# Kernel tuning notes

Measured on AMD Instinct MI355X. Metric: run time of the kernel, lower is better.

Reference implementation:

```python
import jax, jax.numpy as jnp
import numpy as np

B, N_CH, T, E = 64, 64, 1000, 512
KS = [3, 5, 7]
TC, AH, GC, HEADS, NCLS = 16, 32, 32, 4, 2
F3 = TC * len(KS)
EPS = 1e-5


def _gat(x, src, dst, W, a_src, a_dst, bias, N):
    # PyG GATConv, concat=False: h = x @ W.T -> [N, H, C]
    H, C = a_src.shape
    h = (x @ W.T).reshape(-1, H, C)
    al_s = (h * a_src).sum(-1)  # [N, H]
    al_d = (h * a_dst).sum(-1)
    e = al_s[src] + al_d[dst]  # [E, H]
    e = jnp.where(e > 0, e, 0.2 * e)  # leaky_relu(0.2)
    emax = jax.ops.segment_max(e, dst, num_segments=N)
    ex = jnp.exp(e - emax[dst])
    denom = jax.ops.segment_sum(ex, dst, num_segments=N)
    alpha = ex / denom[dst]
    out = jax.ops.segment_sum(h[src] * alpha[:, :, None], dst, num_segments=N)
    return out.mean(1) + bias  # concat=False -> head mean, then bias


def _branch(xr, cw, cb, g, b, m, v, w1, b1, w2, b2):
    k = cw.shape[-1]
    o = jax.lax.conv_general_dilated(xr, cw, (1,), [(k // 2, k // 2)],
                                     dimension_numbers=('NCH', 'OIH', 'NCH'))
    o = o + cb[None, :, None]
    o = (o - m[None, :, None]) / jnp.sqrt(v[None, :, None] + EPS) * g[None, :, None] + b[None, :, None]
    o = jax.nn.gelu(o, approximate=False)
    h = jnp.tanh(jnp.einsum('hc,nct->nht', w1, o) + b1[None, :, None])
    s = jnp.einsum('oh,nht->not', w2, h) + b2[None, :, None]  # [N,1,T]
    wts = jax.nn.softmax(s, axis=2)
    return (o * wts).sum(-1)  # [N, TC]


def reference(x, edge_index,
              conv_w_0, conv_b_0, bn_g_0, bn_b_0, bn_m_0, bn_v_0, aw1_0, ab1_0, aw2_0, ab2_0,
              conv_w_1, conv_b_1, bn_g_1, bn_b_1, bn_m_1, bn_v_1, aw1_1, ab1_1, aw2_1, ab2_1,
              conv_w_2, conv_b_2, bn_g_2, bn_b_2, bn_m_2, bn_v_2, aw1_2, ab1_2, aw2_2, ab2_2,
              se_w1, se_b1, se_w2, se_b2,
              gat1_w, gat1_asrc, gat1_adst, gat1_bias, bn1_g, bn1_b, bn1_m, bn1_v,
              skip_w, skip_b,
              gat2_w, gat2_asrc, gat2_adst, gat2_bias, bn2_g, bn2_b, bn2_m, bn2_v,
              fc_w, fc_b):
    Bx, n, Tn = x.shape
    xr = x.reshape(Bx * n, 1, Tn)
    branches = [
        (conv_w_0, conv_b_0, bn_g_0, bn_b_0, bn_m_0, bn_v_0, aw1_0, ab1_0, aw2_0, ab2_0),
        (conv_w_1, conv_b_1, bn_g_1, bn_b_1, bn_m_1, bn_v_1, aw1_1, ab1_1, aw2_1, ab2_1),
        (conv_w_2, conv_b_2, bn_g_2, bn_b_2, bn_m_2, bn_v_2, aw1_2, ab1_2, aw2_2, ab2_2),
    ]
    feats = [_branch(xr, *p) for p in branches]
    xf = jnp.concatenate(feats, axis=1)  # [B*n, F3]
    # SE block (squeeze over all nodes, per original mean over dim 0)
    sq = xf.mean(0, keepdims=True)
    sq = jax.nn.gelu(sq @ se_w1.T + se_b1, approximate=False)
    sq = jax.nn.sigmoid(sq @ se_w2.T + se_b2)
    xf = xf * sq
    # batched edge index + self loops (PyG GATConv default add_self_loops)
    offs = (jnp.arange(Bx) * n).astype(edge_index.dtype)
    src = (edge_index[0][None, :] + offs[:, None]).reshape(-1)
    dst = (edge_index[1][None, :] + offs[:, None]).reshape(-1)
    loops = jnp.arange(Bx * n, dtype=edge_index.dtype)
    src = jnp.concatenate([src, loops])
    dst = jnp.concatenate([dst, loops])
    Nn = Bx * n
    h1 = _gat(xf, src, dst, gat1_w, gat1_asrc, gat1_adst, gat1_bias, Nn)
    h1 = (h1 - bn1_m) / jnp.sqrt(bn1_v + EPS) * bn1_g + bn1_b
    h1 = jax.nn.gelu(h1 + xf @ skip_w.T + skip_b, approximate=False)
    h2 = _gat(h1, src, dst, gat2_w, gat2_asrc, gat2_adst, gat2_bias, Nn)
    h2 = (h2 - bn2_m) / jnp.sqrt(bn2_v + EPS) * bn2_g + bn2_b
    h2 = jax.nn.gelu(h2 + h1, approximate=False)
    pooled = h2.reshape(Bx, n, -1).mean(1)  # global_mean_pool per graph
    return pooled @ fc_w.T + fc_b


def setup_inputs() -> dict:
    key = jax.random.key(0)
    it = iter(jax.random.split(key, 80))
    nk = lambda *s: jax.random.normal(next(it), s, jnp.float32) * 0.1
    d = {}
    d['x'] = jax.random.normal(next(it), (B, N_CH, T), jnp.float32)
    s0 = jax.random.randint(next(it), (E,), 0, N_CH)
    off = jax.random.randint(next(it), (E,), 1, N_CH)
    d['edge_index'] = jnp.stack([s0, (s0 + off) % N_CH]).astype(jnp.int32)  # no self loops
    for i, k in enumerate(KS):
        d[f'conv_w_{i}'] = nk(TC, 1, k); d[f'conv_b_{i}'] = nk(TC)
        d[f'bn_g_{i}'] = 1.0 + nk(TC); d[f'bn_b_{i}'] = nk(TC)
        d[f'bn_m_{i}'] = nk(TC); d[f'bn_v_{i}'] = 1.0 + jnp.abs(nk(TC))
        d[f'aw1_{i}'] = nk(AH, TC); d[f'ab1_{i}'] = nk(AH)
        d[f'aw2_{i}'] = nk(1, AH); d[f'ab2_{i}'] = nk(1)
    d['se_w1'] = nk(F3 // 4, F3); d['se_b1'] = nk(F3 // 4)
    d['se_w2'] = nk(F3, F3 // 4); d['se_b2'] = nk(F3)
    d['gat1_w'] = nk(HEADS * GC, F3)
    d['gat1_asrc'] = nk(HEADS, GC); d['gat1_adst'] = nk(HEADS, GC); d['gat1_bias'] = nk(GC)
    d['bn1_g'] = 1.0 + nk(GC); d['bn1_b'] = nk(GC); d['bn1_m'] = nk(GC); d['bn1_v'] = 1.0 + jnp.abs(nk(GC))
    d['skip_w'] = nk(GC, F3); d['skip_b'] = nk(GC)
    d['gat2_w'] = nk(HEADS * GC, GC)
    d['gat2_asrc'] = nk(HEADS, GC); d['gat2_adst'] = nk(HEADS, GC); d['gat2_bias'] = nk(GC)
    d['bn2_g'] = 1.0 + nk(GC); d['bn2_b'] = nk(GC); d['bn2_m'] = nk(GC); d['bn2_v'] = 1.0 + jnp.abs(nk(GC))
    d['fc_w'] = nk(NCLS, GC); d['fc_b'] = nk(NCLS)
    return d
```

## Files before the change

kernel.cpp:

```cpp
#include <hip/hip_runtime.h>
#include <math.h>

#define N_NODES 4096
#define T_LEN 1000
#define TCH 16
#define AHD 32
#define F3D 48
#define GCD 32
#define NPG 64
#define NGRAPH 64
#define BN_EPS 1e-5f

typedef _Float16 half4_t __attribute__((ext_vector_type(4)));
typedef float float4_t __attribute__((ext_vector_type(4)));

__device__ __forceinline__ float fast_rcp(float x){ return __builtin_amdgcn_rcpf(x); }
__device__ __forceinline__ float gelu_exact(float v){
    return 0.5f*v*(1.0f+erff(v*0.70710678118654752f));
}

struct BranchParams {
    const float* conv_w; const float* conv_b;
    const float* bn_g; const float* bn_b; const float* bn_m; const float* bn_v;
    const float* aw1; const float* ab1; const float* aw2; const float* ab2;
    int K; int col0;
};

__global__ __launch_bounds__(256)
void branch_kernel(const float* __restrict__ x,
                   BranchParams bp0, BranchParams bp1, BranchParams bp2,
                   float* __restrict__ xf, float* __restrict__ colacc)
{
    __shared__ __align__(16) float xs_f[1056];
    __shared__ __align__(8)  _Float16 xsc[4][1048];
    __shared__ __align__(8)  _Float16 cws16[256];
    __shared__ float s_arr[1024];
    __shared__ __align__(16) float shiftc[16];
    __shared__ float scl[16];
    __shared__ float reds[4];
    __shared__ __align__(16) float fredw[4][16];

    const BranchParams bp = (blockIdx.y==0)? bp0 : (blockIdx.y==1)? bp1 : bp2;
    const int tid = threadIdx.x;
    const int node = blockIdx.x;
    const int K = bp.K;
    const float* xrow = x + (size_t)node*T_LEN;

    for (int j=tid;j<1056;j+=256){
        int q = j-8;
        xs_f[j] = (q>=0 && q<T_LEN)? xrow[q] : 0.f;
    }
    if (tid<16){
        float s = bp.bn_g[tid]*rsqrtf(bp.bn_v[tid]+BN_EPS);
        scl[tid]=s;
        shiftc[tid] = (bp.conv_b[tid]-bp.bn_m[tid])*s + bp.bn_b[tid];
    }
    __syncthreads();
    for (int j=tid;j<1048;j+=256){
        xsc[0][j]=(_Float16)xs_f[j];
        xsc[1][j]=(_Float16)xs_f[j+1];
        xsc[2][j]=(_Float16)xs_f[j+2];
        xsc[3][j]=(_Float16)xs_f[j+3];
    }
    {
        int ch=tid>>4, tap=tid&15;
        cws16[tid] = (tap<K)? (_Float16)(bp.conv_w[ch*K+tap]*scl[ch]) : (_Float16)0.f;
    }
    __syncthreads();

    const int lane = tid&63, wave = tid>>6;
    const int col  = lane&15;
    const int kg   = (lane>>4)<<2;

    const half4_t  acw = *(const half4_t*)&cws16[col*16+kg];
    const float4_t csh = *(const float4_t*)&shiftc[kg];

    const float TWO_LOG2E = 2.8853900817779268f;
    const float LOG2E = 1.4426950408889634f;

    float4_t wr0 = *(const float4_t*)&bp.aw1[(size_t)col*TCH + kg];
    float4_t wr1 = *(const float4_t*)&bp.aw1[(size_t)(col+16)*TCH + kg];
    half4_t a0,a1;
    #pragma unroll
    for (int r=0;r<4;r++){ a0[r]=(_Float16)(wr0[r]*TWO_LOG2E); a1[r]=(_Float16)(wr1[r]*TWO_LOG2E); }
    float4_t c0  = *(const float4_t*)&bp.ab1[kg];
    float4_t c1  = *(const float4_t*)&bp.ab1[16+kg];
    #pragma unroll
    for (int r=0;r<4;r++){ c0[r]*=TWO_LOG2E; c1[r]*=TWO_LOG2E; }
    float4_t w20 = *(const float4_t*)&bp.aw2[kg];
    float4_t w21 = *(const float4_t*)&bp.aw2[16+kg];
    #pragma unroll
    for (int r=0;r<4;r++){ w20[r]*=LOG2E; w21[r]*=LOG2E; }
    const float b2v = bp.ab2[0]*LOG2E;
    const float w2sum8 = w20[0]+w20[1]+w20[2]+w20[3]+w21[0]+w21[1]+w21[2]+w21[3];

    const float C1GE = -2.30220818f;
    const float C2GE = -0.10294324f;

    const int abase = 8 + wave*256 + col + kg - K/2;
    const int sh = abase & 3;
    const _Float16* xw_base = &xsc[sh][abase - sh];

    half4_t oreg[16];
    #pragma unroll
    for (int i=0;i<16;i++){
        half4_t xw = *(const half4_t*)(xw_base + i*16);
        float4_t d = __builtin_amdgcn_mfma_f32_16x16x16f16(acw, xw, csh, 0,0,0);

        float vv[4], dd[4];
        #pragma unroll
        for (int r=0;r<4;r++){
            float v = d[r];
            vv[r] = v;
            float t = fmaxf(v, -9.0f);
            float u = t*t;
            float pq = fmaf(C2GE, u, C1GE);
            dd[r] = __builtin_amdgcn_exp2f(pq*t) + 1.0f;
        }
        half4_t ob;
        {
            float rp0 = fast_rcp(dd[0]*dd[1]);
            float rp1 = fast_rcp(dd[2]*dd[3]);
            ob[0] = (_Float16)(vv[0]*(dd[1]*rp0));
            ob[1] = (_Float16)(vv[1]*(dd[0]*rp0));
            ob[2] = (_Float16)(vv[2]*(dd[3]*rp1));
            ob[3] = (_Float16)(vv[3]*(dd[2]*rp1));
        }
        oreg[i] = ob;

        float4_t h0 = __builtin_amdgcn_mfma_f32_16x16x16f16(a0, ob, c0, 0,0,0);
        float4_t h1 = __builtin_amdgcn_mfma_f32_16x16x16f16(a1, ob, c1, 0,0,0);
        float accr = 0.f;
        #pragma unroll
        for (int r=0;r<4;r++){
            float e0 = __builtin_amdgcn_exp2f(h0[r]) + 1.0f;
            float e1 = __builtin_amdgcn_exp2f(h1[r]) + 1.0f;
            float rp = fast_rcp(e0*e1);
            accr = fmaf(w20[r], e1*rp, accr);
            accr = fmaf(w21[r], e0*rp, accr);
        }
        float part = fmaf(-2.0f, accr, w2sum8);
        part += __shfl_xor(part,16);
        part += __shfl_xor(part,32);
        const int pos0 = wave*256 + i*16;
        if (lane<16) s_arr[pos0+lane] = (pos0+lane < T_LEN)? (part + b2v) : -INFINITY;
    }
    __syncthreads();

    float sv[4];
    #pragma unroll
    for (int ii=0;ii<4;ii++) sv[ii]=s_arr[tid+ii*256];
    float e[4]; float ls=0.f;
    #pragma unroll
    for (int ii=0;ii<4;ii++){ e[ii]=__builtin_amdgcn_exp2f(sv[ii]); ls+=e[ii]; }
    #pragma unroll
    for (int off=32;off;off>>=1) ls += __shfl_xor(ls,off);
    if (lane==0) reds[wave]=ls;
    __syncthreads();
    const float invS = fast_rcp(reds[0]+reds[1]+reds[2]+reds[3]);
    #pragma unroll
    for (int ii=0;ii<4;ii++) s_arr[tid+ii*256]=e[ii];
    __syncthreads();

    half4_t acch = {(_Float16)0.f,(_Float16)0.f,(_Float16)0.f,(_Float16)0.f};
    #pragma unroll
    for (int i=0;i<16;i++){
        _Float16 eh = (_Float16)s_arr[wave*256 + i*16 + col];
        half4_t evv = {eh,eh,eh,eh};
        acch += oreg[i]*evv;
    }
    {
        union { half4_t h; unsigned u[2]; } au, bu;
        au.h = acch;
        #pragma unroll
        for (int off=1;off<16;off<<=1){
            bu.u[0] = __shfl_xor(au.u[0], off);
            bu.u[1] = __shfl_xor(au.u[1], off);
            au.h += bu.h;
        }
        if (col==0){
            float4_t accf;
            #pragma unroll
            for (int r=0;r<4;r++) accf[r] = (float)au.h[r];
            *(float4_t*)&fredw[wave][kg] = accf;
        }
    }
    __syncthreads();
    if (tid<16){
        float v = (fredw[0][tid]+fredw[1][tid]+fredw[2][tid]+fredw[3][tid])*invS;
        xf[(size_t)node*F3D + bp.col0 + tid] = v;
        atomicAdd(&colacc[bp.col0 + tid], v);
    }
}

__global__ __launch_bounds__(128)
void csr_local_kernel(const int* __restrict__ ei, int epg,
                      int* __restrict__ rowstart, int* __restrict__ cols){
    __shared__ int deg[64], cur[64], rs[65];
    const int tid = threadIdx.x;
    if (tid<64) deg[tid]=0;
    __syncthreads();
    const int total = epg + 64;
    for (int e=tid;e<total;e+=128){
        int d = (e<epg)? ei[epg+e] : (e-epg);
        atomicAdd(&deg[d],1);
    }
    __syncthreads();
    if (tid<64){
        int v = deg[tid];
        int s = v;
        #pragma unroll
        for (int off=1;off<64;off<<=1){
            int t = __shfl_up(s, off);
            if (tid >= off) s += t;
        }
        rs[tid+1] = s;
        if (tid==0) rs[0]=0;
        cur[tid] = s - v;
    }
    __syncthreads();
    for (int e=tid;e<total;e+=128){
        int sN,dN;
        if (e<epg){ sN=ei[e]; dN=ei[epg+e]; } else { sN=dN=e-epg; }
        int pos = atomicAdd(&cur[dN],1);
        cols[pos]=sN;
    }
    if (tid<65) rowstart[tid]=rs[tid];
}

__global__ __launch_bounds__(512)
void gat_tail_kernel(const int* __restrict__ rowstart, const int* __restrict__ cols,
                     const float* __restrict__ xf, const float* __restrict__ colacc,
                     const float* __restrict__ se_w1, const float* __restrict__ se_b1,
                     const float* __restrict__ se_w2, const float* __restrict__ se_b2,
                     const float* __restrict__ W1,
                     const float* __restrict__ asrc1, const float* __restrict__ adst1,
                     const float* __restrict__ bias1,
                     const float* __restrict__ bn1_g, const float* __restrict__ bn1_b,
                     const float* __restrict__ bn1_m, const float* __restrict__ bn1_v,
                     const float* __restrict__ skip_w, const float* __restrict__ skip_b,
                     const float* __restrict__ W2,
                     const float* __restrict__ asrc2, const float* __restrict__ adst2,
                     const float* __restrict__ bias2,
                     const float* __restrict__ bn2_g, const float* __restrict__ bn2_b,
                     const float* __restrict__ bn2_m, const float* __restrict__ bn2_v,
                     const float* __restrict__ fc_w, const float* __restrict__ fc_b,
                     float* __restrict__ out)
{
    __shared__ float hb[64*128];
    __shared__ float xh[64*48];
    __shared__ float h1l[64*32];
    __shared__ float a1s[256], a1d[256], a2s[256], a2d[256];
    __shared__ float skw[32*48];
    __shared__ float poolv[32];
    __shared__ float cm[F3D], g1[12], gate_sh[F3D];

    const int g = blockIdx.x;
    const int tid = threadIdx.x;
    const int n0 = g*NPG;

    if (tid<F3D) cm[tid]=colacc[tid]*(1.0f/(float)N_NODES);
    __syncthreads();
    if (tid<12){
        float v=se_b1[tid];
        for (int j=0;j<F3D;j++) v += se_w1[tid*F3D+j]*cm[j];
        g1[tid]=gelu_exact(v);
    }
    __syncthreads();
    if (tid<F3D){
        float v=se_b2[tid];
        for (int m2=0;m2<12;m2++) v += se_w2[tid*12+m2]*g1[m2];
        gate_sh[tid]=fast_rcp(1.0f+__expf(-v));
    }
    __syncthreads();

    for (int i=tid;i<64*48;i+=512)  xh[i] = xf[(size_t)n0*F3D + i] * gate_sh[i%F3D];
    for (int i=tid;i<32*48;i+=512)  skw[i] = skip_w[i];
    __syncthreads();

    for (int i=tid;i<64*128;i+=512){
        const int nl=i>>7, r=i&127;
        const float4* xr=(const float4*)&xh[nl*48];
        const float4* wr=(const float4*)&W1[r*48];
        float acc=0.f;
        #pragma unroll
        for (int j=0;j<12;j++){
            float4 a=xr[j], b=wr[j];
            acc += a.x*b.x + a.y*b.y + a.z*b.z + a.w*b.w;
        }
        hb[i]=acc;
    }
    __syncthreads();

    {
        const int which = tid>>8;
        const int idx = tid&255;
        const int nl=idx>>2, h=idx&3;
        const float* av = which? &adst1[h*32] : &asrc1[h*32];
        const float* hr = &hb[nl*128 + h*32];
        float s=0.f;
        #pragma unroll
        for (int c=0;c<32;c++) s += hr[c]*av[c];
        if (which) a1d[idx]=s; else a1s[idx]=s;
    }
    __syncthreads();

    for (int p=0;p<4;p++){
        const int nl = p*16 + (tid>>5);
        const int c  = tid&31;
        const float4 ad = *(const float4*)&a1d[nl*4];
        float m0=0,m1=0,m2=0,m3=0,d0=0,d1=0,d2=0,d3=0;
        const int s0=rowstart[nl], s1=rowstart[nl+1];
        for (int e=s0;e<s1;e++){
            const int sl = cols[e];
            const float4 as=*(const float4*)&a1s[sl*4];
            float e0=as.x+ad.x; e0=e0>0.f?e0:0.2f*e0; float w0=__expf(e0);
            float e1=as.y+ad.y; e1=e1>0.f?e1:0.2f*e1; float w1=__expf(e1);
            float e2=as.z+ad.z; e2=e2>0.f?e2:0.2f*e2; float w2=__expf(e2);
            float e3=as.w+ad.w; e3=e3>0.f?e3:0.2f*e3; float w3=__expf(e3);
            const float* hr=&hb[sl*128];
            m0+=w0*hr[c]; m1+=w1*hr[32+c]; m2+=w2*hr[64+c]; m3+=w3*hr[96+c];
            d0+=w0; d1+=w1; d2+=w2; d3+=w3;
        }
        float acc = 0.25f*(m0*fast_rcp(d0)+m1*fast_rcp(d1)+m2*fast_rcp(d2)+m3*fast_rcp(d3)) + bias1[c];
        acc = (acc-bn1_m[c])*rsqrtf(bn1_v[c]+BN_EPS)*bn1_g[c]+bn1_b[c];
        float sk = skip_b[c];
        const float* xr=&xh[nl*F3D];
        #pragma unroll
        for (int j=0;j<F3D;j++) sk += xr[j]*skw[c*F3D+j];
        h1l[nl*32+c]=gelu_exact(acc+sk);
    }
    __syncthreads();

    for (int i=tid;i<64*128;i+=512){
        const int nl=i>>7, r=i&127;
        const float4* h1r=(const float4*)&h1l[nl*32];
        const float4* wr =(const float4*)&W2[r*32];
        float acc=0.f;
        #pragma unroll
        for (int j=0;j<8;j++){
            float4 a=h1r[j], b=wr[j];
            acc += a.x*b.x + a.y*b.y + a.z*b.z + a.w*b.w;
        }
        hb[i]=acc;
    }
    __syncthreads();

    {
        const int which = tid>>8;
        const int idx = tid&255;
        const int nl=idx>>2, h=idx&3;
        const float* av = which? &adst2[h*32] : &asrc2[h*32];
        const float* hr = &hb[nl*128 + h*32];
        float s=0.f;
        #pragma unroll
        for (int c=0;c<32;c++) s += hr[c]*av[c];
        if (which) a2d[idx]=s; else a2s[idx]=s;
    }
    __syncthreads();

    for (int p=0;p<4;p++){
        const int nl = p*16 + (tid>>5);
        const int c  = tid&31;
        const float4 ad = *(const float4*)&a2d[nl*4];
        float m0=0,m1=0,m2=0,m3=0,d0=0,d1=0,d2=0,d3=0;
        const int s0=rowstart[nl], s1=rowstart[nl+1];
        for (int e=s0;e<s1;e++){
            const int sl = cols[e];
            const float4 as=*(const float4*)&a2s[sl*4];
            float e0=as.x+ad.x; e0=e0>0.f?e0:0.2f*e0; float w0=__expf(e0);
            float e1=as.y+ad.y; e1=e1>0.f?e1:0.2f*e1; float w1=__expf(e1);
            float e2=as.z+ad.z; e2=e2>0.f?e2:0.2f*e2; float w2=__expf(e2);
            float e3=as.w+ad.w; e3=e3>0.f?e3:0.2f*e3; float w3=__expf(e3);
            const float* hr=&hb[sl*128];
            m0+=w0*hr[c]; m1+=w1*hr[32+c]; m2+=w2*hr[64+c]; m3+=w3*hr[96+c];
            d0+=w0; d1+=w1; d2+=w2; d3+=w3;
        }
        float acc = 0.25f*(m0*fast_rcp(d0)+m1*fast_rcp(d1)+m2*fast_rcp(d2)+m3*fast_rcp(d3)) + bias2[c];
        acc = (acc-bn2_m[c])*rsqrtf(bn2_v[c]+BN_EPS)*bn2_g[c]+bn2_b[c];
        float v = acc + h1l[nl*32+c];
        xh[nl*32+c]=gelu_exact(v);
    }
    __syncthreads();

    if (tid<32){
        float s=0.f;
        for (int n=0;n<NPG;n++) s += xh[n*32+tid];
        poolv[tid]=s*(1.0f/(float)NPG);
    }
    __syncthreads();
    if (tid<2){
        float o=fc_b[tid];
        #pragma unroll
        for (int c=0;c<GCD;c++) o += poolv[c]*fc_w[tid*GCD+c];
        out[g*2+tid]=o;
    }
}

extern "C" void kernel_launch(void* const* d_in, const int* in_sizes, int n_in,
                              void* d_out, int out_size, void* d_ws, size_t ws_size,
                              hipStream_t stream){
    const float* x = (const float*)d_in[0];
    const int* ei = (const int*)d_in[1];
    const int epg = in_sizes[1]/2;

    float* ws = (float*)d_ws;
    float* xf      = ws;
    float* colacc  = xf + (size_t)N_NODES*F3D;
    int*   rowstart = (int*)(colacc + 64);
    int*   cols     = rowstart + 80;

    auto P = [&](int i){ return (const float*)d_in[i]; };

    (void)hipMemsetAsync(colacc, 0, 64*sizeof(float), stream);
    csr_local_kernel<<<1,128,0,stream>>>(ei,epg,rowstart,cols);

    BranchParams bps[3];
    const int Ks[3] = {3,5,7};
    for (int b=0;b<3;b++){
        int base = 2 + b*10;
        bps[b].conv_w = P(base+0); bps[b].conv_b = P(base+1);
        bps[b].bn_g = P(base+2);   bps[b].bn_b = P(base+3);
        bps[b].bn_m = P(base+4);   bps[b].bn_v = P(base+5);
        bps[b].aw1 = P(base+6);    bps[b].ab1 = P(base+7);
        bps[b].aw2 = P(base+8);    bps[b].ab2 = P(base+9);
        bps[b].K = Ks[b]; bps[b].col0 = b*TCH;
    }
    branch_kernel<<<dim3(N_NODES,3),256,0,stream>>>(x, bps[0], bps[1], bps[2], xf, colacc);

    gat_tail_kernel<<<NGRAPH,512,0,stream>>>(
        rowstart,cols,
        xf,colacc,P(32),P(33),P(34),P(35),
        P(36),P(37),P(38),
        P(39),P(40),P(41),P(42),P(43),
        P(44),P(45),
        P(46),P(47),P(48),P(49),P(50),P(51),P(52),P(53),
        P(54),P(55),(float*)d_out);
}
```

Before: 232.0 us.

## Fold CSR build and column-mean into GAT tail kernel, drop memset and atomics

Removes the separate CSR-building kernel and the memset, and rebuilds the per-graph CSR in shared memory inside each GAT tail block. The branch kernel no longer does a global atomicAdd per output to build column sums. Instead, every tail block reduces the full xf matrix (4096x48) itself using vectorised loads and wave shuffles. This cuts two launches and 12k contended atomics, at the cost of each of the 64 tail blocks redundantly reading about 786KB of xf.

```diff
diff --git a/kernel.cpp b/kernel.cpp
--- a/kernel.cpp
+++ b/kernel.cpp
@@ -29,7 +29,7 @@
 __global__ __launch_bounds__(256)
 void branch_kernel(const float* __restrict__ x,
                    BranchParams bp0, BranchParams bp1, BranchParams bp2,
-                   float* __restrict__ xf, float* __restrict__ colacc)
+                   float* __restrict__ xf)
 {
     __shared__ __align__(16) float xs_f[1056];
     __shared__ __align__(8)  _Float16 xsc[4][1048];
@@ -189,48 +189,12 @@
     if (tid<16){
         float v = (fredw[0][tid]+fredw[1][tid]+fredw[2][tid]+fredw[3][tid])*invS;
         xf[(size_t)node*F3D + bp.col0 + tid] = v;
-        atomicAdd(&colacc[bp.col0 + tid], v);
     }
 }
 
-__global__ __launch_bounds__(128)
-void csr_local_kernel(const int* __restrict__ ei, int epg,
-                      int* __restrict__ rowstart, int* __restrict__ cols){
-    __shared__ int deg[64], cur[64], rs[65];
-    const int tid = threadIdx.x;
-    if (tid<64) deg[tid]=0;
-    __syncthreads();
-    const int total = epg + 64;
-    for (int e=tid;e<total;e+=128){
-        int d = (e<epg)? ei[epg+e] : (e-epg);
-        atomicAdd(&deg[d],1);
-    }
-    __syncthreads();
-    if (tid<64){
-        int v = deg[tid];
-        int s = v;
-        #pragma unroll
-        for (int off=1;off<64;off<<=1){
-            int t = __shfl_up(s, off);
-            if (tid >= off) s += t;
-        }
-        rs[tid+1] = s;
-        if (tid==0) rs[0]=0;
-        cur[tid] = s - v;
-    }
-    __syncthreads();
-    for (int e=tid;e<total;e+=128){
-        int sN,dN;
-        if (e<epg){ sN=ei[e]; dN=ei[epg+e]; } else { sN=dN=e-epg; }
-        int pos = atomicAdd(&cur[dN],1);
-        cols[pos]=sN;
-    }
-    if (tid<65) rowstart[tid]=rs[tid];
-}
-
 __global__ __launch_bounds__(512)
-void gat_tail_kernel(const int* __restrict__ rowstart, const int* __restrict__ cols,
-                     const float* __restrict__ xf, const float* __restrict__ colacc,
+void gat_tail_kernel(const int* __restrict__ ei, int epg,
+                     const float* __restrict__ xf,
                      const float* __restrict__ se_w1, const float* __restrict__ se_b1,
                      const float* __restrict__ se_w2, const float* __restrict__ se_b2,
                      const float* __restrict__ W1,
@@ -254,13 +218,75 @@
     __shared__ float skw[32*48];
     __shared__ float poolv[32];
     __shared__ float cm[F3D], g1[12], gate_sh[F3D];
+    __shared__ float wred[8][F3D];
+    __shared__ int   deg[64], cur[64], rsl[65];
+    __shared__ int   colsl[1152];
 
     const int g = blockIdx.x;
     const int tid = threadIdx.x;
+    const int lane = tid&63, wave = tid>>6;
     const int n0 = g*NPG;
-
-    if (tid<F3D) cm[tid]=colacc[tid]*(1.0f/(float)N_NODES);
-    __syncthreads();
+    const int etot = epg + 64;
+
+    if (tid<64) deg[tid]=0;
+    __syncthreads();
+    for (int e=tid;e<etot;e+=512){
+        int d = (e<epg)? ei[epg+e] : (e-epg);
+        atomicAdd(&deg[d],1);
+    }
+    __syncthreads();
+    if (tid<64){
+        int v = deg[tid];
+        int s = v;
+        #pragma unroll
+        for (int off=1;off<64;off<<=1){
+            int t = __shfl_up(s, off);
+            if (lane >= off) s += t;
+        }
+        rsl[tid+1] = s;
+        if (tid==0) rsl[0]=0;
+        cur[tid] = s - v;
+    }
+    __syncthreads();
+    for (int e=tid;e<etot;e+=512){
+        int sN,dN;
+        if (e<epg){ sN=ei[e]; dN=ei[epg+e]; } else { sN=dN=e-epg; }
+        int pos = atomicAdd(&cur[dN],1);
+        colsl[pos]=sN;
+    }
+
+    {
+        float4_t accv[12];
+        #pragma unroll
+        for (int j=0;j<12;j++) accv[j] = (float4_t){0.f,0.f,0.f,0.f};
+        const float4_t* xf4 = (const float4_t*)xf;
+        const int base = tid*96;
+        #pragma unroll
+        for (int k=0;k<96;k++) accv[k%12] += xf4[base+k];
+        #pragma unroll
+        for (int j=0;j<12;j++){
+            #pragma unroll
+            for (int off=1;off<64;off<<=1){
+                accv[j][0] += __shfl_xor(accv[j][0], off);
+                accv[j][1] += __shfl_xor(accv[j][1], off);
+                accv[j][2] += __shfl_xor(accv[j][2], off);
+                accv[j][3] += __shfl_xor(accv[j][3], off);
+            }
+        }
+        if (lane==0){
+            #pragma unroll
+            for (int j=0;j<12;j++) *(float4_t*)&wred[wave][j*4] = accv[j];
+        }
+    }
+    __syncthreads();
+    if (tid<F3D){
+        float s=0.f;
+        #pragma unroll
+        for (int w=0;w<8;w++) s += wred[w][tid];
+        cm[tid] = s*(1.0f/(float)N_NODES);
+    }
+    __syncthreads();
+
     if (tid<12){
         float v=se_b1[tid];
         for (int j=0;j<F3D;j++) v += se_w1[tid*F3D+j]*cm[j];
@@ -310,9 +336,9 @@
         const int c  = tid&31;
         const float4 ad = *(const float4*)&a1d[nl*4];
         float m0=0,m1=0,m2=0,m3=0,d0=0,d1=0,d2=0,d3=0;
-        const int s0=rowstart[nl], s1=rowstart[nl+1];
+        const int s0=rsl[nl], s1=rsl[nl+1];
         for (int e=s0;e<s1;e++){
-            const int sl = cols[e];
+            const int sl = colsl[e];
             const float4 as=*(const float4*)&a1s[sl*4];
             float e0=as.x+ad.x; e0=e0>0.f?e0:0.2f*e0; float w0=__expf(e0);
             float e1=as.y+ad.y; e1=e1>0.f?e1:0.2f*e1; float w1=__expf(e1);
@@ -364,9 +390,9 @@
         const int c  = tid&31;
         const float4 ad = *(const float4*)&a2d[nl*4];
         float m0=0,m1=0,m2=0,m3=0,d0=0,d1=0,d2=0,d3=0;
-        const int s0=rowstart[nl], s1=rowstart[nl+1];
+        const int s0=rsl[nl], s1=rsl[nl+1];
         for (int e=s0;e<s1;e++){
-            const int sl = cols[e];
+            const int sl = colsl[e];
             const float4 as=*(const float4*)&a2s[sl*4];
             float e0=as.x+ad.x; e0=e0>0.f?e0:0.2f*e0; float w0=__expf(e0);
             float e1=as.y+ad.y; e1=e1>0.f?e1:0.2f*e1; float w1=__expf(e1);
@@ -404,16 +430,9 @@
     const int* ei = (const int*)d_in[1];
     const int epg = in_sizes[1]/2;
 
-    float* ws = (float*)d_ws;
-    float* xf      = ws;
-    float* colacc  = xf + (size_t)N_NODES*F3D;
-    int*   rowstart = (int*)(colacc + 64);
-    int*   cols     = rowstart + 80;
+    float* xf = (float*)d_ws;
 
     auto P = [&](int i){ return (const float*)d_in[i]; };
-
-    (void)hipMemsetAsync(colacc, 0, 64*sizeof(float), stream);
-    csr_local_kernel<<<1,128,0,stream>>>(ei,epg,rowstart,cols);
 
     BranchParams bps[3];
     const int Ks[3] = {3,5,7};
@@ -426,11 +445,11 @@
         bps[b].aw2 = P(base+8);    bps[b].ab2 = P(base+9);
         bps[b].K = Ks[b]; bps[b].col0 = b*TCH;
     }
-    branch_kernel<<<dim3(N_NODES,3),256,0,stream>>>(x, bps[0], bps[1], bps[2], xf, colacc);
+    branch_kernel<<<dim3(N_NODES,3),256,0,stream>>>(x, bps[0], bps[1], bps[2], xf);
 
     gat_tail_kernel<<<NGRAPH,512,0,stream>>>(
-        rowstart,cols,
-        xf,colacc,P(32),P(33),P(34),P(35),
+        ei, epg, xf,
+        P(32),P(33),P(34),P(35),
         P(36),P(37),P(38),
         P(39),P(40),P(41),P(42),P(43),
         P(44),P(45),
```

Measured after the change: 242.5 us. +4.5%, slower.
